# Performance work log

Hardware: AMD Instinct MI355X
Metric: run time of the kernel (lower is better)

## Reference

```python
import jax, jax.numpy as jnp
import numpy as np

B, H, N, D = 16, 8, 256, 32


def setup_inputs() -> dict:
    key = jax.random.key(0)
    k1, k2, k3 = jax.random.split(key, 3)
    q = jax.random.normal(k1, (B, H, N, D), dtype=jnp.float32)
    k = jax.random.normal(k2, (B, H, N, D), dtype=jnp.float32)
    scale = jnp.ones((1,), dtype=jnp.float32)  # unused by the module
    mask = jnp.zeros((B, 1, N, N), dtype=bool)  # True == masked out
    # learned attention vector, xavier_uniform over (1, H, 1, 1, D)
    fan = 1 * H * 1 * 1 * D
    bound = float(np.sqrt(6.0 / (1 + D)))  # xavier for (..., D) param
    attention = jax.random.uniform(k3, (1, H, 1, 1, D), dtype=jnp.float32,
                                   minval=-bound, maxval=bound)
    return {"q": q, "k": k, "scale": scale, "mask": mask, "attention": attention}


def reference(q, k, scale, mask, attention):
    # summed: [B, H, Nq, Nk, D] via broadcast of q.unsqueeze(-2)+k.unsqueeze(-3)
    summed = q[:, :, :, None, :] + k[:, :, None, :, :]
    # GATv2 score: a^T * silu(q_i + k_j), reduced over head_dim
    scores = jnp.sum(jax.nn.silu(summed) * attention, axis=-1)  # [B, H, Nq, Nk]
    neg = jnp.finfo(scores.dtype).min
    scores_masked = jnp.where(mask, neg, scores)
    attn = jax.nn.softmax(scores_masked, axis=-1)
    return attn
```

## Files before the change

### kernel.cpp

```cpp
#include <hip/hip_runtime.h>
#include <stdint.h>
#include <stddef.h>

constexpr int Bc = 16, Hc = 8, Nc = 256, Dc = 32;
constexpr float LOG2E = 1.44269504088896340736f;

constexpr int    MF    = 10;
constexpr double PHALF = 9.7;
constexpr double LFIT  = 9.0;

constexpr double PI_ = 3.14159265358979323846;

constexpr double cexp_(double x) {
    int n = (int)(x >= 0 ? x + 0.5 : x - 0.5);
    double f = x - n, t = 1.0, s = 1.0;
    for (int i = 1; i <= 26; ++i) { t *= f / i; s += t; }
    const double E = 2.71828182845904523536;
    double en = 1.0, bb = n >= 0 ? E : 1.0 / E;
    int an = n < 0 ? -n : n;
    for (int i = 0; i < an; ++i) en *= bb;
    return s * en;
}
constexpr double creduce_(double x) {
    while (x >  PI_) x -= 2.0 * PI_;
    while (x < -PI_) x += 2.0 * PI_;
    return x;
}
constexpr double ccos_(double x0) {
    double x = creduce_(x0), x2 = x * x, t = 1.0, s = 1.0;
    for (int i = 1; i <= 16; ++i) { t *= -x2 / ((2.0*i - 1.0) * (2.0*i)); s += t; }
    return s;
}
constexpr double csin_(double x0) {
    double x = creduce_(x0), x2 = x * x, t = x, s = x;
    for (int i = 1; i <= 16; ++i) { t *= -x2 / ((2.0*i) * (2.0*i + 1.0)); s += t; }
    return s;
}
constexpr double Gfun_(double x) {
    double z = x < 0 ? -x : x;
    double e = cexp_(z);
    return 0.5 * z * ((e - 1.0) / (e + 1.0));
}
constexpr double csqrt_(double x) {
    if (x <= 0) return 0;
    double r = x > 1 ? x : 1;
    for (int i = 0; i < 40; ++i) r = 0.5 * (r + x / r);
    return r;
}

struct FitT { float tk[MF + 1]; float tq[MF + 1]; };

constexpr FitT lsFit_() {
    constexpr int NB = MF + 1;
    double A[NB][NB] = {}, bv[NB] = {};
    for (int p = 0; p < NB; ++p)
        for (int qq = 0; qq < NB; ++qq) {
            double wm = (p - qq) * PI_ / PHALF, wp = (p + qq) * PI_ / PHALF;
            double Sm = (p == qq)     ? LFIT : csin_(wm * LFIT) / wm;
            double Sp = (p + qq == 0) ? LFIT : csin_(wp * LFIT) / wp;
            A[p][qq] = 0.5 * (Sm + Sp);
        }
    constexpr int NS = 128;
    double hh = LFIT / NS, gx[NS + 1] = {};
    for (int i = 0; i <= NS; ++i) gx[i] = Gfun_(i * hh);
    for (int p = 0; p < NB; ++p) {
        double s = 0;
        for (int i = 0; i <= NS; ++i) {
            double wgt = (i == 0 || i == NS) ? 1.0 : ((i & 1) ? 4.0 : 2.0);
            s += wgt * gx[i] * ccos_(p * PI_ / PHALF * (i * hh));
        }
        bv[p] = s * hh / 3.0;
    }
    for (int p = 0; p < NB; ++p) A[p][p] += 1e-8 * LFIT;
    for (int col = 0; col < NB; ++col) {
        int piv = col; double best = A[col][col] < 0 ? -A[col][col] : A[col][col];
        for (int r = col + 1; r < NB; ++r) {
            double v = A[r][col] < 0 ? -A[r][col] : A[r][col];
            if (v > best) { best = v; piv = r; }
        }
        if (piv != col) {
            for (int cc = 0; cc < NB; ++cc) { double t = A[col][cc]; A[col][cc] = A[piv][cc]; A[piv][cc] = t; }
            double t = bv[col]; bv[col] = bv[piv]; bv[piv] = t;
        }
        for (int r = col + 1; r < NB; ++r) {
            double f = A[r][col] / A[col][col];
            for (int cc = col; cc < NB; ++cc) A[r][cc] -= f * A[col][cc];
            bv[r] -= f * bv[col];
        }
    }
    double c[NB] = {};
    for (int r = NB - 1; r >= 0; --r) {
        double s = bv[r];
        for (int cc = r + 1; cc < NB; ++cc) s -= A[r][cc] * c[cc];
        c[r] = s / A[r][r];
    }
    FitT f{};
    for (int m = 0; m <= MF; ++m) {
        double rt = csqrt_(c[m] < 0 ? -c[m] : c[m]);
        f.tk[m] = (float)rt;
        f.tq[m] = (float)(c[m] < 0 ? -rt : rt);
    }
    return f;
}
constexpr FitT CF = lsFit_();

typedef _Float16 half8  __attribute__((ext_vector_type(8)));
typedef float    f32x16 __attribute__((ext_vector_type(16)));

__device__ __forceinline__ uint32_t pkh_(float a, float b) {
    auto v = __builtin_amdgcn_cvt_pkrtz(a, b);
    uint32_t u; __builtin_memcpy(&u, &v, 4); return u;
}

constexpr int KB_  = Nc * 128;
constexpr int QB_  = 128 * 128;
constexpr int BUF  = KB_ + QB_;
constexpr int SRED_OFF = 2 * BUF;
constexpr int AKV_OFF  = SRED_OFF + 2048;
constexpr int SMEM     = AKV_OFF + 1024;

__global__ __launch_bounds__(1024, 4) void gatv2_mfma_kernel(
    const float* __restrict__ q, const float* __restrict__ k,
    const uint8_t* __restrict__ mask, const float* __restrict__ att,
    float* __restrict__ out)
{
    extern __shared__ char smem[];
    float* sred = (float*)(smem + SRED_OFF);
    float* akv  = (float*)(smem + AKV_OFF);

    const int tid = threadIdx.x, lane = tid & 63, w = tid >> 6;
    const int bh = blockIdx.y, h = bh & 7, b = bh >> 3;
    const int iBlk = blockIdx.x * 128;
    const float invTwoP = (float)(1.0 / (2.0 * PHALF));

    const int dq = tid & 7, rw = tid >> 3;
    const float4 a4 = *(const float4*)(att + h * Dc + 4 * dq);
    const int swS = (dq ^ (rw & 7)) << 4;

    const float* kbase = k + (size_t)bh * Nc * Dc;
    float kc1[8], ks1[8], kcm[8], ksm[8];
    int offK[2];
#pragma unroll
    for (int it = 0; it < 2; ++it) {
        const int j = rw + it * 128;
        const float4 kv = *(const float4*)(kbase + j * Dc + 4 * dq);
        float part = a4.x * kv.x + a4.y * kv.y + a4.z * kv.z + a4.w * kv.w;
        part += __shfl_xor(part, 1, 64);
        part += __shfl_xor(part, 2, 64);
        part += __shfl_xor(part, 4, 64);
        if (dq == 0) akv[j] = part;
        const float rv[4] = { kv.x, kv.y, kv.z, kv.w };
#pragma unroll
        for (int c = 0; c < 4; ++c) {
            float r = __builtin_amdgcn_fractf(rv[c] * invTwoP);
            kc1[4*it+c] = __builtin_amdgcn_cosf(r);
            ks1[4*it+c] = __builtin_amdgcn_sinf(r);
            kcm[4*it+c] = kc1[4*it+c];
            ksm[4*it+c] = ks1[4*it+c];
        }
        offK[it] = j * 128 + swS;
    }
    const float* qbase = q + ((size_t)bh * Nc + iBlk) * Dc;
    float qc1[4], qs1[4], qcm[4], qsm[4];
    const int offQ = KB_ + rw * 128 + swS;
    {
        const float4 qv = *(const float4*)(qbase + rw * Dc + 4 * dq);
        const float rv[4] = { qv.x, qv.y, qv.z, qv.w };
#pragma unroll
        for (int c = 0; c < 4; ++c) {
            float r = __builtin_amdgcn_fractf(rv[c] * invTwoP);
            qc1[c] = __builtin_amdgcn_cosf(r);
            qs1[c] = __builtin_amdgcn_sinf(r);
            qcm[c] = qc1[c]; qsm[c] = qs1[c];
        }
    }

    const int hi5 = lane >> 5, col = lane & 31;
    const int wi = w & 3, wj = w >> 2;
    const int baseA  = KB_ + (wi * 32 + col) * 128;
    const int baseB0 = (wj * 64 + col) * 128, baseB1 = baseB0 + 32 * 128;
    const int sA = col & 7;

    f32x16 acc[2];
#pragma unroll
    for (int jt = 0; jt < 2; ++jt)
#pragma unroll
        for (int e = 0; e < 16; ++e) acc[jt][e] = 0.0f;

    auto buildChunk = [&](int m, int dstOff) {
        const float tk = CF.tk[m];
        const float g0 = CF.tq[m]*a4.x, g1 = CF.tq[m]*a4.y;
        const float g2 = CF.tq[m]*a4.z, g3 = CF.tq[m]*a4.w;
#pragma unroll
        for (int it = 0; it < 2; ++it) {
            uint4 wv;
            wv.x = pkh_(tk * kcm[4*it+0], tk * ksm[4*it+0]);
            wv.y = pkh_(tk * kcm[4*it+1], tk * ksm[4*it+1]);
            wv.z = pkh_(tk * kcm[4*it+2], tk * ksm[4*it+2]);
            wv.w = pkh_(tk * kcm[4*it+3], tk * ksm[4*it+3]);
            *(uint4*)(smem + dstOff + offK[it]) = wv;
        }
        {
            uint4 wv;
            wv.x = pkh_(g0 * qcm[0], -(g0 * qsm[0]));
            wv.y = pkh_(g1 * qcm[1], -(g1 * qsm[1]));
            wv.z = pkh_(g2 * qcm[2], -(g2 * qsm[2]));
            wv.w = pkh_(g3 * qcm[3], -(g3 * qsm[3]));
            *(uint4*)(smem + dstOff + offQ) = wv;
        }
        if (m < MF) {
#pragma unroll
            for (int e = 0; e < 8; ++e) {
                float cn = fmaf(kc1[e], kcm[e], -(ks1[e] * ksm[e]));
                float sn = fmaf(ks1[e], kcm[e],   kc1[e] * ksm[e]);
                kcm[e] = cn; ksm[e] = sn;
            }
#pragma unroll
            for (int e = 0; e < 4; ++e) {
                float cn = fmaf(qc1[e], qcm[e], -(qs1[e] * qsm[e]));
                float sn = fmaf(qs1[e], qcm[e],   qc1[e] * qsm[e]);
                qcm[e] = cn; qsm[e] = sn;
            }
        }
    };

    auto mfmaChunk = [&](int srcOff) {
#pragma unroll
        for (int s = 0; s < 4; ++s) {
            const int du = ((2 * s + hi5) ^ sA) << 4;
            half8 A  = *(const half8*)(smem + srcOff + baseA  + du);
            half8 B0 = *(const half8*)(smem + srcOff + baseB0 + du);
            half8 B1 = *(const half8*)(smem + srcOff + baseB1 + du);
            acc[0] = __builtin_amdgcn_mfma_f32_32x32x16_f16(A, B0, acc[0], 0, 0, 0);
            acc[1] = __builtin_amdgcn_mfma_f32_32x32x16_f16(A, B1, acc[1], 0, 0, 0);
        }
    };

    buildChunk(1, 0);
    __syncthreads();
#pragma unroll
    for (int m = 1; m <= MF; ++m) {
        if (m < MF) buildChunk(m + 1, (m & 1) * BUF);
        mfmaChunk(((m - 1) & 1) * BUF);
        __syncthreads();
    }

    constexpr float M0 = 24.0f;
    const int jB = wj * 64;
    const float akj0 = akv[jB + col], akj1 = akv[jB + 32 + col];
    const int iB = iBlk + wi * 32;

#pragma unroll
    for (int e = 0; e < 16; ++e) {
        int rloc = (e & 3) + 8 * (e >> 2) + 4 * hi5;
        int ig = iB + rloc;
        const uint8_t* mr = mask + ((size_t)(b * Nc + ig)) * Nc + jB + col;
        float v0 = fmaf(0.5f, akj0, acc[0][e]);
        float v1 = fmaf(0.5f, akj1, acc[1][e]);
        if (mr[0])  v0 = -1.0e30f;
        if (mr[32]) v1 = -1.0e30f;
        float p0 = __builtin_amdgcn_exp2f(__builtin_fminf((v0 - M0) * LOG2E, 80.0f));
        float p1 = __builtin_amdgcn_exp2f(__builtin_fminf((v1 - M0) * LOG2E, 80.0f));
        acc[0][e] = p0;
        acc[1][e] = p1;
        float sm = p0 + p1;
#pragma unroll
        for (int off = 1; off < 32; off <<= 1) sm += __shfl_xor(sm, off, 64);
        if (col == e) sred[(wi * 32 + rloc) * 4 + wj] = sm;
    }
    __syncthreads();

    float* obase = out + (size_t)bh * Nc * Nc;
#pragma unroll
    for (int e = 0; e < 16; ++e) {
        int rloc = (e & 3) + 8 * (e >> 2) + 4 * hi5;
        int iL = wi * 32 + rloc;
        int ig = iB + rloc;
        float4 tv = *(const float4*)(&sred[iL * 4]);
        float inv = __builtin_amdgcn_rcpf(tv.x + tv.y + tv.z + tv.w);
        obase[(size_t)ig * Nc + jB + col]      = acc[0][e] * inv;
        obase[(size_t)ig * Nc + jB + 32 + col] = acc[1][e] * inv;
    }
}

extern "C" void kernel_launch(void* const* d_in, const int* in_sizes, int n_in,
                              void* d_out, int out_size, void* d_ws, size_t ws_size,
                              hipStream_t stream) {
    const float*   q    = (const float*)d_in[0];
    const float*   k    = (const float*)d_in[1];
    const uint8_t* mask = (const uint8_t*)d_in[3];
    const float*   att  = (const float*)d_in[4];
    float*         out  = (float*)d_out;

    (void)hipFuncSetAttribute((const void*)gatv2_mfma_kernel,
                              hipFuncAttributeMaxDynamicSharedMemorySize, SMEM);

    dim3 grid(2, Bc * Hc);
    dim3 block(1024);
    gatv2_mfma_kernel<<<grid, block, SMEM, stream>>>(q, k, mask, att, out);
}
```

Before: 98.65 us.

## Halve query tile per block, single-buffer LDS, recompute harmonics with direct sin/cos

Each block now handles 64 query rows with 512 threads, so the grid doubles to 4 x B*H blocks. The LDS double buffer is dropped for a single buffer with two barriers per harmonic. The cos/sin recurrence is replaced by direct fract/cos/sin evaluation of m*theta for every harmonic. The aim is more blocks in flight and a smaller LDS footprint for better occupancy. In exchange, build and MFMA no longer overlap, each thread issues more transcendental instructions, and the K build work is repeated by twice as many blocks.

```diff
diff --git a/kernel.cpp b/kernel.cpp
--- a/kernel.cpp
+++ b/kernel.cpp
@@ -113,13 +113,12 @@
 }
 
 constexpr int KB_  = Nc * 128;
-constexpr int QB_  = 128 * 128;
-constexpr int BUF  = KB_ + QB_;
-constexpr int SRED_OFF = 2 * BUF;
-constexpr int AKV_OFF  = SRED_OFF + 2048;
+constexpr int QB_  = 64 * 128;
+constexpr int SRED_OFF = KB_ + QB_;
+constexpr int AKV_OFF  = SRED_OFF + 1024;
 constexpr int SMEM     = AKV_OFF + 1024;
 
-__global__ __launch_bounds__(1024, 4) void gatv2_mfma_kernel(
+__global__ __launch_bounds__(512, 4) void gatv2_mfma_kernel(
     const float* __restrict__ q, const float* __restrict__ k,
     const uint8_t* __restrict__ mask, const float* __restrict__ att,
     float* __restrict__ out)
@@ -130,7 +129,7 @@
 
     const int tid = threadIdx.x, lane = tid & 63, w = tid >> 6;
     const int bh = blockIdx.y, h = bh & 7, b = bh >> 3;
-    const int iBlk = blockIdx.x * 128;
+    const int iBlk = blockIdx.x * 64;
     const float invTwoP = (float)(1.0 / (2.0 * PHALF));
 
     const int dq = tid & 7, rw = tid >> 3;
@@ -138,45 +137,33 @@
     const int swS = (dq ^ (rw & 7)) << 4;
 
     const float* kbase = k + (size_t)bh * Nc * Dc;
-    float kc1[8], ks1[8], kcm[8], ksm[8];
-    int offK[2];
-#pragma unroll
-    for (int it = 0; it < 2; ++it) {
-        const int j = rw + it * 128;
+    float tK[16];
+    int offK[4];
+#pragma unroll
+    for (int it = 0; it < 4; ++it) {
+        const int j = rw + it * 64;
         const float4 kv = *(const float4*)(kbase + j * Dc + 4 * dq);
         float part = a4.x * kv.x + a4.y * kv.y + a4.z * kv.z + a4.w * kv.w;
         part += __shfl_xor(part, 1, 64);
         part += __shfl_xor(part, 2, 64);
         part += __shfl_xor(part, 4, 64);
         if (dq == 0) akv[j] = part;
-        const float rv[4] = { kv.x, kv.y, kv.z, kv.w };
-#pragma unroll
-        for (int c = 0; c < 4; ++c) {
-            float r = __builtin_amdgcn_fractf(rv[c] * invTwoP);
-            kc1[4*it+c] = __builtin_amdgcn_cosf(r);
-            ks1[4*it+c] = __builtin_amdgcn_sinf(r);
-            kcm[4*it+c] = kc1[4*it+c];
-            ksm[4*it+c] = ks1[4*it+c];
-        }
+        tK[4*it+0] = kv.x * invTwoP;
+        tK[4*it+1] = kv.y * invTwoP;
+        tK[4*it+2] = kv.z * invTwoP;
+        tK[4*it+3] = kv.w * invTwoP;
         offK[it] = j * 128 + swS;
     }
-    const float* qbase = q + ((size_t)bh * Nc + iBlk) * Dc;
-    float qc1[4], qs1[4], qcm[4], qsm[4];
+    float tQ[4];
     const int offQ = KB_ + rw * 128 + swS;
     {
-        const float4 qv = *(const float4*)(qbase + rw * Dc + 4 * dq);
-        const float rv[4] = { qv.x, qv.y, qv.z, qv.w };
-#pragma unroll
-        for (int c = 0; c < 4; ++c) {
-            float r = __builtin_amdgcn_fractf(rv[c] * invTwoP);
-            qc1[c] = __builtin_amdgcn_cosf(r);
-            qs1[c] = __builtin_amdgcn_sinf(r);
-            qcm[c] = qc1[c]; qsm[c] = qs1[c];
-        }
+        const float4 qv = *(const float4*)(q + ((size_t)bh * Nc + iBlk + rw) * Dc + 4 * dq);
+        tQ[0] = qv.x * invTwoP; tQ[1] = qv.y * invTwoP;
+        tQ[2] = qv.z * invTwoP; tQ[3] = qv.w * invTwoP;
     }
 
     const int hi5 = lane >> 5, col = lane & 31;
-    const int wi = w & 3, wj = w >> 2;
+    const int wi = w & 1, wj = w >> 1;
     const int baseA  = KB_ + (wi * 32 + col) * 128;
     const int baseB0 = (wj * 64 + col) * 128, baseB1 = baseB0 + 32 * 128;
     const int sA = col & 7;
@@ -187,61 +174,61 @@
 #pragma unroll
         for (int e = 0; e < 16; ++e) acc[jt][e] = 0.0f;
 
-    auto buildChunk = [&](int m, int dstOff) {
+    auto buildChunk = [&](int m) {
+        const float fm = (float)m;
         const float tk = CF.tk[m];
         const float g0 = CF.tq[m]*a4.x, g1 = CF.tq[m]*a4.y;
         const float g2 = CF.tq[m]*a4.z, g3 = CF.tq[m]*a4.w;
 #pragma unroll
-        for (int it = 0; it < 2; ++it) {
+        for (int it = 0; it < 4; ++it) {
+            float cc[4], ss[4];
+#pragma unroll
+            for (int c = 0; c < 4; ++c) {
+                float ang = __builtin_amdgcn_fractf(fm * tK[4*it+c]);
+                cc[c] = __builtin_amdgcn_cosf(ang);
+                ss[c] = __builtin_amdgcn_sinf(ang);
+            }
             uint4 wv;
-            wv.x = pkh_(tk * kcm[4*it+0], tk * ksm[4*it+0]);
-            wv.y = pkh_(tk * kcm[4*it+1], tk * ksm[4*it+1]);
-            wv.z = pkh_(tk * kcm[4*it+2], tk * ksm[4*it+2]);
-            wv.w = pkh_(tk * kcm[4*it+3], tk * ksm[4*it+3]);
-            *(uint4*)(smem + dstOff + offK[it]) = wv;
+            wv.x = pkh_(tk * cc[0], tk * ss[0]);
+            wv.y = pkh_(tk * cc[1], tk * ss[1]);
+            wv.z = pkh_(tk * cc[2], tk * ss[2]);
+            wv.w = pkh_(tk * cc[3], tk * ss[3]);
+            *(uint4*)(smem + offK[it]) = wv;
         }
         {
+            float cc[4], ss[4];
+#pragma unroll
+            for (int c = 0; c < 4; ++c) {
+                float ang = __builtin_amdgcn_fractf(fm * tQ[c]);
+                cc[c] = __builtin_amdgcn_cosf(ang);
+                ss[c] = __builtin_amdgcn_sinf(ang);
+            }
             uint4 wv;
-            wv.x = pkh_(g0 * qcm[0], -(g0 * qsm[0]));
-            wv.y = pkh_(g1 * qcm[1], -(g1 * qsm[1]));
-            wv.z = pkh_(g2 * qcm[2], -(g2 * qsm[2]));
-            wv.w = pkh_(g3 * qcm[3], -(g3 * qsm[3]));
-            *(uint4*)(smem + dstOff + offQ) = wv;
-        }
-        if (m < MF) {
-#pragma unroll
-            for (int e = 0; e < 8; ++e) {
-                float cn = fmaf(kc1[e], kcm[e], -(ks1[e] * ksm[e]));
-                float sn = fmaf(ks1[e], kcm[e],   kc1[e] * ksm[e]);
-                kcm[e] = cn; ksm[e] = sn;
-            }
-#pragma unroll
-            for (int e = 0; e < 4; ++e) {
-                float cn = fmaf(qc1[e], qcm[e], -(qs1[e] * qsm[e]));
-                float sn = fmaf(qs1[e], qcm[e],   qc1[e] * qsm[e]);
-                qcm[e] = cn; qsm[e] = sn;
-            }
+            wv.x = pkh_(g0 * cc[0], -(g0 * ss[0]));
+            wv.y = pkh_(g1 * cc[1], -(g1 * ss[1]));
+            wv.z = pkh_(g2 * cc[2], -(g2 * ss[2]));
+            wv.w = pkh_(g3 * cc[3], -(g3 * ss[3]));
+            *(uint4*)(smem + offQ) = wv;
         }
     };
 
-    auto mfmaChunk = [&](int srcOff) {
+    auto mfmaChunk = [&]() {
 #pragma unroll
         for (int s = 0; s < 4; ++s) {
             const int du = ((2 * s + hi5) ^ sA) << 4;
-            half8 A  = *(const half8*)(smem + srcOff + baseA  + du);
-            half8 B0 = *(const half8*)(smem + srcOff + baseB0 + du);
-            half8 B1 = *(const half8*)(smem + srcOff + baseB1 + du);
+            half8 A  = *(const half8*)(smem + baseA  + du);
+            half8 B0 = *(const half8*)(smem + baseB0 + du);
+            half8 B1 = *(const half8*)(smem + baseB1 + du);
             acc[0] = __builtin_amdgcn_mfma_f32_32x32x16_f16(A, B0, acc[0], 0, 0, 0);
             acc[1] = __builtin_amdgcn_mfma_f32_32x32x16_f16(A, B1, acc[1], 0, 0, 0);
         }
     };
 
-    buildChunk(1, 0);
-    __syncthreads();
 #pragma unroll
     for (int m = 1; m <= MF; ++m) {
-        if (m < MF) buildChunk(m + 1, (m & 1) * BUF);
-        mfmaChunk(((m - 1) & 1) * BUF);
+        buildChunk(m);
+        __syncthreads();
+        mfmaChunk();
         __syncthreads();
     }
 
@@ -295,7 +282,7 @@
     (void)hipFuncSetAttribute((const void*)gatv2_mfma_kernel,
                               hipFuncAttributeMaxDynamicSharedMemorySize, SMEM);
 
-    dim3 grid(2, Bc * Hc);
-    dim3 block(1024);
+    dim3 grid(4, Bc * Hc);
+    dim3 block(512);
     gatv2_mfma_kernel<<<grid, block, SMEM, stream>>>(q, k, mask, att, out);
 }
```

Result: slower. 104.6 us (+6.1%).
